# Optimization experiments

Hardware: AMD Instinct MI355X
Metric: run time of the kernel (lower is better)

The kernel has to match this reference:

```python
import jax, jax.numpy as jnp
import numpy as np

B, S, E2, E = 2, 512, 512, 256  # batch, seq, 2*encode_size, encode_size


def setup_inputs() -> dict:
    key = jax.random.key(0)
    k1, k2, k3, k4 = jax.random.split(key, 4)
    query = jax.random.normal(k1, (B, S, E2), dtype=jnp.float32)
    value = jax.random.normal(k2, (B, S, E2), dtype=jnp.float32)
    # nn.Linear weights (no bias); stored as [in, out] for x @ W convention
    Wd = jax.random.normal(k3, (E2, E), dtype=jnp.float32) * (1.0 / np.sqrt(E2))
    vd = jax.random.normal(k4, (E,), dtype=jnp.float32) * (1.0 / np.sqrt(E))
    return {"query": query, "value": value, "Wd": Wd, "vd": vd}


def reference(query, value, Wd, vd):
    # q = query.unsqueeze(1) -> [B,1,S,2E]; k = query.unsqueeze(2) -> [B,S,1,2E]
    # NOTE: original module ignores its `key` arg; both factors come from query.
    qk = query[:, None, :, :] * query[:, :, None, :]        # [B,S,S,2E]
    h = jnp.tanh(jnp.einsum('bsth,hd->bstd', qk, Wd))        # [B,S,S,E]
    sjt = jnp.einsum('bstd,d->bst', h, vd)                   # [B,S,S]
    atten = jax.nn.softmax(sjt, axis=2)                      # softmax over dim=2
    # dropout p=0.0 -> identity
    context = jnp.einsum('bst,btd->bsd', atten, value)       # bmm
    return (context, atten)
```

## Files before the change

kernel.cpp:

```cpp
#include <hip/hip_runtime.h>

#define B_  2
#define S_  512
#define E2_ 512
#define E_  256

#define TT  128
#define KB  32
#define LDK 40

using f32x4 = __attribute__((ext_vector_type(4))) float;
using f16x8 = __attribute__((ext_vector_type(8))) _Float16;

__device__ __forceinline__ float tanh_fast(float x) {
    float e = __expf(2.0f * x);
    return 1.0f - 2.0f / (e + 1.0f);
}

__device__ __forceinline__ void gld16(const void* g, void* l) {
    __builtin_amdgcn_global_load_lds(
        (const __attribute__((address_space(1))) unsigned int*)g,
        (__attribute__((address_space(3))) unsigned int*)l, 16, 0, 0);
}

#define SBAR() __builtin_amdgcn_sched_barrier(0)

__global__ void prep_wdt(const float* __restrict__ Wd, _Float16* __restrict__ Wp) {
    int idx = blockIdx.x * 256 + threadIdx.x;
    int h = idx >> 8;
    int d = idx & 255;
    int ko = h >> 5;
    int kk = h & 31;
    Wp[(size_t)ko * (E_ * LDK) + d * LDK + kk] = (_Float16)Wd[idx];
}

__global__ __launch_bounds__(512, 4)
void stage1(const float* __restrict__ q,
            const _Float16* __restrict__ Wp,
            const float* __restrict__ vd,
            float* __restrict__ logits ) {
    const int p  = blockIdx.x >> 7;
    const int sl = blockIdx.x & 127;
    const int b  = blockIdx.y;
    const int sj = (p >= 6) ? 3 : (p >= 3) ? 2 : (p >= 1) ? 1 : 0;
    const int ti = p - ((sj * (sj + 1)) >> 1);
    const int s  = sj * TT + sl;
    const int t0 = ti * TT;

    __shared__ _Float16 sA[2][TT * LDK];
    __shared__ _Float16 sB[2][E_ * LDK];
    __shared__ float sQs[E2_];
    __shared__ float sVd[E_];

    const int tid = threadIdx.x;
    {
        const float* qsrow = q + ((size_t)(b * S_ + s)) * E2_;
        sQs[tid] = qsrow[tid];
        if (tid < E_) sVd[tid] = vd[tid];
    }
    __syncthreads();

    const int wave = tid >> 6;
    const int lane = tid & 63;
    const int wt   = wave >> 2;
    const int wd   = wave & 3;
    const int l15  = lane & 15;
    const int l4   = lane >> 4;

    const int a_row = tid >> 2;
    const int a_g   = tid & 3;
    const int a_off = a_row * LDK + a_g * 8;
    const float* qt = q + ((size_t)(b * S_ + t0 + a_row)) * E2_ + a_g * 8;

    const char* wsrc = (const char*)Wp + wave * 1024 + lane * 16;
    const int   ldst = wave * 1024;

    float4 ra0, ra1;
    auto ALOAD = [&](int k0) {
        ra0 = *(const float4*)(qt + k0);
        ra1 = *(const float4*)(qt + k0 + 4);
    };
    auto AWRITE = [&](int k0, int h) {
        const float* qq = &sQs[k0 + a_g * 8];
        float4 q0 = *(const float4*)(qq);
        float4 q1 = *(const float4*)(qq + 4);
        f16x8 hv;
        hv[0] = (_Float16)(ra0.x * q0.x); hv[1] = (_Float16)(ra0.y * q0.y);
        hv[2] = (_Float16)(ra0.z * q0.z); hv[3] = (_Float16)(ra0.w * q0.w);
        hv[4] = (_Float16)(ra1.x * q1.x); hv[5] = (_Float16)(ra1.y * q1.y);
        hv[6] = (_Float16)(ra1.z * q1.z); hv[7] = (_Float16)(ra1.w * q1.w);
        *(f16x8*)&sA[h][a_off] = hv;
    };
    auto BDMA = [&](int ko, int h) {
        const char* src = wsrc + ko * 20480;
        char* dst = (char*)&sB[h][0] + ldst;
        gld16(src,        dst);
        gld16(src + 8192, dst + 8192);
        if (wave < 4) gld16(src + 16384, dst + 16384);
    };

    f32x4 acc[4][4] = {};

    ALOAD(0);
    SBAR();
    AWRITE(0, 0);
    SBAR();
    BDMA(0, 0);
    SBAR();
    ALOAD(KB);
    SBAR();
    asm volatile("s_waitcnt vmcnt(2) lgkmcnt(0)" ::: "memory");
    __builtin_amdgcn_s_barrier();

    for (int ko = 0; ko < E2_ / KB; ++ko) {
        const int h = ko & 1;
        f16x8 af[4], bf[4];
#pragma unroll
        for (int ft = 0; ft < 4; ++ft) {
            int row = wt * 64 + ft * 16 + l15;
            af[ft] = *(const f16x8*)&sA[h][row * LDK + l4 * 8];
        }
#pragma unroll
        for (int fd = 0; fd < 4; ++fd) {
            int row = wd * 64 + fd * 16 + l15;
            bf[fd] = *(const f16x8*)&sB[h][row * LDK + l4 * 8];
        }
        SBAR();
        if (ko < 15) {
            AWRITE((ko + 1) * KB, h ^ 1);
            SBAR();
            BDMA(ko + 1, h ^ 1);
        }
        SBAR();
        if (ko < 14) {
            ALOAD((ko + 2) * KB);
            SBAR();
            asm volatile("s_waitcnt vmcnt(2) lgkmcnt(0)" ::: "memory");
            __builtin_amdgcn_s_barrier();
        } else if (ko < 15) {
            asm volatile("s_waitcnt vmcnt(0) lgkmcnt(0)" ::: "memory");
            __builtin_amdgcn_s_barrier();
        }
        __builtin_amdgcn_s_setprio(1);
#pragma unroll
        for (int ft = 0; ft < 4; ++ft) {
#pragma unroll
            for (int fd = 0; fd < 4; ++fd) {
                acc[ft][fd] = __builtin_amdgcn_mfma_f32_16x16x32_f16(af[ft], bf[fd], acc[ft][fd], 0, 0, 0);
            }
        }
        __builtin_amdgcn_s_setprio(0);
    }

    __syncthreads();

    float* sRed = (float*)&sA[0][0];
    {
        float vdr[4];
#pragma unroll
        for (int fd = 0; fd < 4; ++fd) vdr[fd] = sVd[wd * 64 + fd * 16 + l15];
#pragma unroll
        for (int ft = 0; ft < 4; ++ft) {
#pragma unroll
            for (int r = 0; r < 4; ++r) {
                float pp = 0.f;
#pragma unroll
                for (int fd = 0; fd < 4; ++fd)
                    pp += tanh_fast(acc[ft][fd][r]) * vdr[fd];
                pp += __shfl_xor(pp, 1);
                pp += __shfl_xor(pp, 2);
                pp += __shfl_xor(pp, 4);
                pp += __shfl_xor(pp, 8);
                if (l15 == 0) {
                    int tl = wt * 64 + ft * 16 + l4 * 4 + r;
                    sRed[tl * 4 + wd] = pp;
                }
            }
        }
    }
    __syncthreads();
    if (tid < TT) {
        float v = sRed[tid * 4 + 0] + sRed[tid * 4 + 1] + sRed[tid * 4 + 2] + sRed[tid * 4 + 3];
        int t = t0 + tid;
        logits[((size_t)(b * S_ + s)) * S_ + t] = v;
        logits[((size_t)(b * S_ + t)) * S_ + s] = v;
    }
}

__global__ void softmax_k(float* __restrict__ atten) {
    const int row  = blockIdx.x;
    const int lane = threadIdx.x;
    float* p = atten + (size_t)row * S_;
    float4 v0 = *(float4*)(p + lane * 8);
    float4 v1 = *(float4*)(p + lane * 8 + 4);
    float vv[8] = {v0.x, v0.y, v0.z, v0.w, v1.x, v1.y, v1.z, v1.w};
    float m = vv[0];
#pragma unroll
    for (int j = 1; j < 8; ++j) m = fmaxf(m, vv[j]);
#pragma unroll
    for (int off = 1; off < 64; off <<= 1) m = fmaxf(m, __shfl_xor(m, off));
    float ssum = 0.f;
#pragma unroll
    for (int j = 0; j < 8; ++j) { vv[j] = __expf(vv[j] - m); ssum += vv[j]; }
#pragma unroll
    for (int off = 1; off < 64; off <<= 1) ssum += __shfl_xor(ssum, off);
    float inv = 1.0f / ssum;
    float4 o0 = {vv[0] * inv, vv[1] * inv, vv[2] * inv, vv[3] * inv};
    float4 o1 = {vv[4] * inv, vv[5] * inv, vv[6] * inv, vv[7] * inv};
    *(float4*)(p + lane * 8)     = o0;
    *(float4*)(p + lane * 8 + 4) = o1;
}

__global__ __launch_bounds__(256)
void context_k(const float* __restrict__ atten, const float* __restrict__ value,
               float* __restrict__ ctx) {
    __shared__ float sA[32][65];
    __shared__ float sV[64][65];
    const int b  = blockIdx.z;
    const int s0 = blockIdx.y * 32;
    const int e0 = blockIdx.x * 64;
    const int tid = threadIdx.x;
    const int ts = tid >> 4;
    const int te = tid & 15;

    float acc[2][4] = {};
    for (int k0 = 0; k0 < S_; k0 += 64) {
        {
            int r = tid >> 3;
            int c = (tid & 7) * 8;
            const float* ga = atten + ((size_t)(b * S_ + s0 + r)) * S_ + k0 + c;
            *(float4*)&sA[r][c]     = *(const float4*)ga;
            *(float4*)&sA[r][c + 4] = *(const float4*)(ga + 4);
        }
        {
            int r = tid >> 2;
            int c = (tid & 3) * 16;
            const float* gv = value + ((size_t)(b * S_ + k0 + r)) * E2_ + e0 + c;
#pragma unroll
            for (int j = 0; j < 16; j += 4)
                *(float4*)&sV[r][c + j] = *(const float4*)(gv + j);
        }
        __syncthreads();
#pragma unroll 8
        for (int kk = 0; kk < 64; ++kk) {
            float a0 = sA[ts * 2 + 0][kk];
            float a1 = sA[ts * 2 + 1][kk];
#pragma unroll
            for (int j = 0; j < 4; ++j) {
                float vvv = sV[kk][te * 4 + j];
                acc[0][j] += a0 * vvv;
                acc[1][j] += a1 * vvv;
            }
        }
        __syncthreads();
    }
#pragma unroll
    for (int i = 0; i < 2; ++i)
#pragma unroll
        for (int j = 0; j < 4; ++j)
            ctx[((size_t)(b * S_ + s0 + ts * 2 + i)) * E2_ + e0 + te * 4 + j] = acc[i][j];
}

extern "C" void kernel_launch(void* const* d_in, const int* in_sizes, int n_in,
                              void* d_out, int out_size, void* d_ws, size_t ws_size,
                              hipStream_t stream) {
    const float* query = (const float*)d_in[0];
    const float* value = (const float*)d_in[1];
    const float* Wd    = (const float*)d_in[2];
    const float* vd    = (const float*)d_in[3];

    float* out   = (float*)d_out;
    float* ctx   = out;
    float* atten = out + (size_t)B_ * S_ * E2_;

    const size_t wdt_bytes = (size_t)16 * E_ * LDK * sizeof(_Float16);
    _Float16* wp;
    if (ws_size >= wdt_bytes) {
        wp = (_Float16*)d_ws;
    } else {
        wp = (_Float16*)ctx;
    }

    prep_wdt<<<dim3(512), dim3(256), 0, stream>>>(Wd, wp);
    stage1<<<dim3(1280, B_), dim3(512), 0, stream>>>(query, wp, vd, atten);
    softmax_k<<<dim3(B_ * S_), dim3(64), 0, stream>>>(atten);
    context_k<<<dim3(E2_ / 64, S_ / 32, B_), dim3(256), 0, stream>>>(atten, value, ctx);
}
```

Measured before the change: 168.4 us.

## Load Wd fragments directly from global into registers, drop LDS staging

The B operand (transposed fp16 Wd) is now packed unpadded and each wave reads its MFMA fragments straight from global/L2 into registers every k-step, instead of DMA-ing tiles into a double-buffered LDS array. This removes the sB shared buffer, the global_load_lds traffic and its vmcnt waits, which cuts LDS footprint and may raise occupancy. In exchange every wave issues global loads on the critical path right before the MFMAs, with no prefetch, so latency could be exposed. Redundant reads across waves now rely on cache hits.

```diff
diff --git a/kernel.cpp b/kernel.cpp
--- a/kernel.cpp
+++ b/kernel.cpp
@@ -17,26 +17,20 @@
     return 1.0f - 2.0f / (e + 1.0f);
 }
 
-__device__ __forceinline__ void gld16(const void* g, void* l) {
-    __builtin_amdgcn_global_load_lds(
-        (const __attribute__((address_space(1))) unsigned int*)g,
-        (__attribute__((address_space(3))) unsigned int*)l, 16, 0, 0);
-}
-
 #define SBAR() __builtin_amdgcn_sched_barrier(0)
 
-__global__ void prep_wdt(const float* __restrict__ Wd, _Float16* __restrict__ Wp) {
+__global__ void prep_wdt(const float* __restrict__ Wd, _Float16* __restrict__ Wp2) {
     int idx = blockIdx.x * 256 + threadIdx.x;
     int h = idx >> 8;
     int d = idx & 255;
     int ko = h >> 5;
     int kk = h & 31;
-    Wp[(size_t)ko * (E_ * LDK) + d * LDK + kk] = (_Float16)Wd[idx];
+    Wp2[ko * (E_ * KB) + d * KB + kk] = (_Float16)Wd[idx];
 }
 
 __global__ __launch_bounds__(512, 4)
 void stage1(const float* __restrict__ q,
-            const _Float16* __restrict__ Wp,
+            const _Float16* __restrict__ Wp2,
             const float* __restrict__ vd,
             float* __restrict__ logits ) {
     const int p  = blockIdx.x >> 7;
@@ -48,7 +42,6 @@
     const int t0 = ti * TT;
 
     __shared__ _Float16 sA[2][TT * LDK];
-    __shared__ _Float16 sB[2][E_ * LDK];
     __shared__ float sQs[E2_];
     __shared__ float sVd[E_];
 
@@ -72,8 +65,7 @@
     const int a_off = a_row * LDK + a_g * 8;
     const float* qt = q + ((size_t)(b * S_ + t0 + a_row)) * E2_ + a_g * 8;
 
-    const char* wsrc = (const char*)Wp + wave * 1024 + lane * 16;
-    const int   ldst = wave * 1024;
+    const _Float16* wpb = Wp2 + (wd * 64 + l15) * KB + l4 * 8;
 
     float4 ra0, ra1;
     auto ALOAD = [&](int k0) {
@@ -91,13 +83,6 @@
         hv[6] = (_Float16)(ra1.z * q1.z); hv[7] = (_Float16)(ra1.w * q1.w);
         *(f16x8*)&sA[h][a_off] = hv;
     };
-    auto BDMA = [&](int ko, int h) {
-        const char* src = wsrc + ko * 20480;
-        char* dst = (char*)&sB[h][0] + ldst;
-        gld16(src,        dst);
-        gld16(src + 8192, dst + 8192);
-        if (wave < 4) gld16(src + 16384, dst + 16384);
-    };
 
     f32x4 acc[4][4] = {};
 
@@ -105,41 +90,41 @@
     SBAR();
     AWRITE(0, 0);
     SBAR();
-    BDMA(0, 0);
-    SBAR();
     ALOAD(KB);
     SBAR();
-    asm volatile("s_waitcnt vmcnt(2) lgkmcnt(0)" ::: "memory");
+    asm volatile("s_waitcnt lgkmcnt(0)" ::: "memory");
     __builtin_amdgcn_s_barrier();
+    SBAR();
 
     for (int ko = 0; ko < E2_ / KB; ++ko) {
         const int h = ko & 1;
-        f16x8 af[4], bf[4];
+        f16x8 bf[4];
+        {
+            const _Float16* wk = wpb + ko * (E_ * KB);
+#pragma unroll
+            for (int fd = 0; fd < 4; ++fd)
+                bf[fd] = *(const f16x8*)(wk + fd * 16 * KB);
+        }
+        SBAR();
+        f16x8 af[4];
 #pragma unroll
         for (int ft = 0; ft < 4; ++ft) {
             int row = wt * 64 + ft * 16 + l15;
             af[ft] = *(const f16x8*)&sA[h][row * LDK + l4 * 8];
-        }
-#pragma unroll
-        for (int fd = 0; fd < 4; ++fd) {
-            int row = wd * 64 + fd * 16 + l15;
-            bf[fd] = *(const f16x8*)&sB[h][row * LDK + l4 * 8];
         }
         SBAR();
         if (ko < 15) {
             AWRITE((ko + 1) * KB, h ^ 1);
             SBAR();
-            BDMA(ko + 1, h ^ 1);
-        }
-        SBAR();
+        }
         if (ko < 14) {
             ALOAD((ko + 2) * KB);
             SBAR();
-            asm volatile("s_waitcnt vmcnt(2) lgkmcnt(0)" ::: "memory");
+        }
+        if (ko < 15) {
+            asm volatile("s_waitcnt lgkmcnt(0)" ::: "memory");
             __builtin_amdgcn_s_barrier();
-        } else if (ko < 15) {
-            asm volatile("s_waitcnt vmcnt(0) lgkmcnt(0)" ::: "memory");
-            __builtin_amdgcn_s_barrier();
+            SBAR();
         }
         __builtin_amdgcn_s_setprio(1);
 #pragma unroll
@@ -273,16 +258,16 @@
     float* ctx   = out;
     float* atten = out + (size_t)B_ * S_ * E2_;
 
-    const size_t wdt_bytes = (size_t)16 * E_ * LDK * sizeof(_Float16);
-    _Float16* wp;
+    const size_t wdt_bytes = (size_t)16 * E_ * KB * sizeof(_Float16);
+    _Float16* wp2;
     if (ws_size >= wdt_bytes) {
-        wp = (_Float16*)d_ws;
+        wp2 = (_Float16*)d_ws;
     } else {
-        wp = (_Float16*)ctx;
-    }
-
-    prep_wdt<<<dim3(512), dim3(256), 0, stream>>>(Wd, wp);
-    stage1<<<dim3(1280, B_), dim3(512), 0, stream>>>(query, wp, vd, atten);
+        wp2 = (_Float16*)ctx;
+    }
+
+    prep_wdt<<<dim3(512), dim3(256), 0, stream>>>(Wd, wp2);
+    stage1<<<dim3(1280, B_), dim3(512), 0, stream>>>(query, wp2, vd, atten);
     softmax_k<<<dim3(B_ * S_), dim3(64), 0, stream>>>(atten);
     context_k<<<dim3(E2_ / 64, S_ / 32, B_), dim3(256), 0, stream>>>(atten, value, ctx);
 }
```

Measured after the change: 160.1 us. -4.9%, faster.
